# Kernel tuning notes

Measured on AMD Instinct MI355X. Metric: run time of the kernel, lower is better.

## Reference

```python
import jax, jax.numpy as jnp
import numpy as np


def setup_inputs() -> dict:
    key = jax.random.key(0)
    k1, k2 = jax.random.split(key)
    B, C, H, W = 8, 64, 32, 32
    K = 8192
    x = jax.random.normal(k1, (B, C, H, W), dtype=jnp.float32)
    codebook = jax.random.normal(k2, (K, C), dtype=jnp.float32)
    return {"x": x, "codebook": codebook}


def reference(x, codebook):
    """Faithful JAX version of VQVAE.quantize().

    x:        [B, C, H, W] latent (output of pre_quant_conv)
    codebook: [K, C] embedding weight
    Returns (quant_out [B,C,H,W], commitment_loss, codebook_loss, indices [B,H,W]).
    """
    B, C, H, W = x.shape
    # [B, H, W, C] -> [B, N, C]
    xf = jnp.transpose(x, (0, 2, 3, 1)).reshape(B, H * W, C)

    # Squared pairwise distances (argmin of cdist == argmin of squared dist).
    x2 = jnp.sum(xf * xf, axis=-1, keepdims=True)            # [B, N, 1]
    e2 = jnp.sum(codebook * codebook, axis=-1)               # [K]
    xe = jnp.einsum('bnc,kc->bnk', xf, codebook)             # [B, N, K]
    d2 = x2 + e2[None, None, :] - 2.0 * xe                   # [B, N, K]
    idx = jnp.argmin(d2, axis=-1)                            # [B, N]

    quant = codebook[idx.reshape(-1)]                        # [B*N, C]
    xflat = xf.reshape(-1, C)                                # [B*N, C]

    commitment_loss = jnp.mean((jax.lax.stop_gradient(quant) - xflat) ** 2)
    codebook_loss = jnp.mean((quant - jax.lax.stop_gradient(xflat)) ** 2)

    # Straight-through estimator.
    quant_st = xflat + jax.lax.stop_gradient(quant - xflat)
    quant_out = jnp.transpose(quant_st.reshape(B, H, W, C), (0, 3, 1, 2))
    indices = idx.reshape(B, H, W)
    return quant_out, commitment_loss, codebook_loss, indices
```

## Files before the change

kernel.cpp:

```cpp
#include <hip/hip_runtime.h>


#define N_PTS   8192
#define K_CODES 8192
#define C_DIM   64
#define HWSZ    1024
#define QOUT_N  524288
#define SPLITS  16

#define WS_XS    0
#define WS_CBS   2097152
#define WS_E2H   4194304
#define WS_PACK  4227072
#define WS_PART  5275648

typedef __attribute__((ext_vector_type(8))) short    short8;
typedef __attribute__((ext_vector_type(8))) _Float16 half8;
typedef __attribute__((ext_vector_type(4))) float    floatx4;

__device__ __forceinline__ half8 as_h8(short8 v) {
    return __builtin_bit_cast(half8, v);
}
__device__ __forceinline__ void split2(float v, unsigned short& h,
                                       unsigned short& m) {
    _Float16 hh = (_Float16)v;
    float r = v - (float)hh;
    _Float16 mm = (_Float16)r;
    h = __builtin_bit_cast(unsigned short, hh);
    m = __builtin_bit_cast(unsigned short, mm);
}
__device__ __forceinline__ void cp16(const void* g, void* l) {
    __builtin_amdgcn_global_load_lds(
        (const __attribute__((address_space(1))) void*)g,
        (__attribute__((address_space(3))) void*)l, 16, 0, 0);
}
__device__ __forceinline__ void cp4(const void* g, void* l) {
    __builtin_amdgcn_global_load_lds(
        (const __attribute__((address_space(1))) void*)g,
        (__attribute__((address_space(3))) void*)l, 4, 0, 0);
}

__global__ __launch_bounds__(256)
void vq_prep_kernel(const float* __restrict__ x,
                    const float* __restrict__ cb,
                    unsigned short* __restrict__ xS,
                    unsigned short* __restrict__ cbS,
                    float* __restrict__ e2h)
{
    const int bx  = blockIdx.x;
    const int tid = threadIdx.x;

    if (bx < 32) {
        const int k = bx * 256 + tid;
        const float* row = cb + k * C_DIM;
        float s = 0.0f;
        #pragma unroll
        for (int g = 0; g < 8; ++g) {
            float4 a = *(const float4*)(row + g * 8);
            float4 b = *(const float4*)(row + g * 8 + 4);
            float vv[8] = {a.x, a.y, a.z, a.w, b.x, b.y, b.z, b.w};
            unsigned short h8[8], m8[8];
            #pragma unroll
            for (int j = 0; j < 8; ++j) {
                s = fmaf(vv[j], vv[j], s);
                split2(vv[j], h8[j], m8[j]);
            }
            *(uint4*)(cbS + ((size_t)(0 * 8 + g) * 8192 + k) * 8) = *(const uint4*)h8;
            *(uint4*)(cbS + ((size_t)(1 * 8 + g) * 8192 + k) * 8) = *(const uint4*)m8;
        }
        e2h[k] = 0.5f * s;
    } else {
        const int u = bx - 32;
        const int b = u >> 5, g = (u >> 2) & 7, q = u & 3;
        const int hw = q * 256 + tid;
        const float* xb = x + (size_t)(b * C_DIM + g * 8) * HWSZ + hw;
        unsigned short h8[8], m8[8];
        #pragma unroll
        for (int cq = 0; cq < 8; ++cq)
            split2(xb[cq * HWSZ], h8[cq], m8[cq]);
        const size_t n = (size_t)b * 1024 + hw;
        *(uint4*)(xS + ((size_t)(0 * 8 + g) * 8192 + n) * 8) = *(const uint4*)h8;
        *(uint4*)(xS + ((size_t)(1 * 8 + g) * 8192 + n) * 8) = *(const uint4*)m8;
    }
}

#define SEG_SHORTS 512
#define NSEGS      16
#define BUF_SHORTS 8320

__device__ __forceinline__ void computeTile(const half8 af[4][2][2],
                                            const unsigned short* __restrict__ bsrc,
                                            int tl, int quad, int col, int code,
                                            float bestv[4][4], int besti[4][4])
{
    half8 bf[2][2];
    #pragma unroll
    for (int p = 0; p < 2; ++p)
        #pragma unroll
        for (int s = 0; s < 2; ++s) {
            int seg = p * 8 + s * 4 + quad;
            bf[p][s] = as_h8(*(const short8*)(bsrc + seg * SEG_SHORTS + (tl * 16 + col) * 8));
        }
    float me2 = -((const float*)(bsrc + NSEGS * SEG_SHORTS))[tl * 16 + col];

    floatx4 acc[4];
    #pragma unroll
    for (int t = 0; t < 4; ++t) acc[t] = (floatx4){me2, me2, me2, me2};

    #pragma unroll
    for (int s = 0; s < 2; ++s) {
        #pragma unroll
        for (int t = 0; t < 4; ++t)
            acc[t] = __builtin_amdgcn_mfma_f32_16x16x32_f16(af[t][0][s], bf[0][s], acc[t], 0, 0, 0);
        #pragma unroll
        for (int t = 0; t < 4; ++t)
            acc[t] = __builtin_amdgcn_mfma_f32_16x16x32_f16(af[t][0][s], bf[1][s], acc[t], 0, 0, 0);
        #pragma unroll
        for (int t = 0; t < 4; ++t)
            acc[t] = __builtin_amdgcn_mfma_f32_16x16x32_f16(af[t][1][s], bf[0][s], acc[t], 0, 0, 0);
    }

    #pragma unroll
    for (int t = 0; t < 4; ++t)
        #pragma unroll
        for (int r = 0; r < 4; ++r) {
            float sc = acc[t][r];
            bool gt = sc > bestv[t][r];
            bestv[t][r] = gt ? sc   : bestv[t][r];
            besti[t][r] = gt ? code : besti[t][r];
        }
}

__global__ __launch_bounds__(512, 1)
void vq_argmin_kernel(const unsigned short* __restrict__ xS,
                      const unsigned short* __restrict__ cbS,
                      const float* __restrict__ e2h,
                      unsigned long long* __restrict__ packedS)
{
    __shared__ __align__(16) unsigned short sBuf[2][BUF_SHORTS];

    const int tid   = threadIdx.x;
    const int lane  = tid & 63;
    const int w     = tid >> 6;
    const int col   = lane & 15;
    const int quad  = lane >> 4;
    const int mb    = blockIdx.x;
    const int split = blockIdx.y;
    const int m0    = mb * 512 + w * 64;
    const int nb0   = split * 512;

    half8 af[4][2][2];
    #pragma unroll
    for (int t = 0; t < 4; ++t) {
        int pt = m0 + t * 16 + col;
        #pragma unroll
        for (int p = 0; p < 2; ++p)
            #pragma unroll
            for (int s = 0; s < 2; ++s) {
                int g = s * 4 + quad;
                af[t][p][s] = as_h8(*(const short8*)(xS + ((size_t)(p * 8 + g) * 8192 + pt) * 8));
            }
    }

    float bestv[4][4];
    int   besti[4][4];
    #pragma unroll
    for (int t = 0; t < 4; ++t)
        #pragma unroll
        for (int r = 0; r < 4; ++r) {
            bestv[t][r] = __uint_as_float(0xFF800000u);
            besti[t][r] = 0;
        }

    auto stage = [&](int k0, int buf) {
        unsigned short* dst = &sBuf[buf][0];
        #pragma unroll
        for (int i = 0; i < 2; ++i) {
            int f   = tid + i * 512;
            int seg = f >> 6;
            int l   = f & 63;
            cp16(cbS + ((size_t)seg * 8192 + k0 + l) * 8,
                 dst + seg * SEG_SHORTS + l * 8);
        }
        if (tid < 64)
            cp4(e2h + k0 + tid, (float*)(dst + NSEGS * SEG_SHORTS) + tid);
    };

    stage(nb0, 0);
    __syncthreads();

    for (int ch = 0; ch < 8; ++ch) {
        if (ch + 1 < 8) stage(nb0 + (ch + 1) * 64, (ch + 1) & 1);
        const unsigned short* bsrc = &sBuf[ch & 1][0];
        #pragma unroll
        for (int tl = 0; tl < 4; ++tl)
            computeTile(af, bsrc, tl, quad, col,
                        nb0 + ch * 64 + tl * 16 + col, bestv, besti);
        __syncthreads();
    }

    unsigned long long own = 0;
    #pragma unroll
    for (int t = 0; t < 4; ++t)
        #pragma unroll
        for (int r = 0; r < 4; ++r) {
            unsigned u = __float_as_uint(-bestv[t][r]);
            u = ((int)u < 0) ? ~u : (u | 0x80000000u);
            unsigned long long p = ((unsigned long long)u << 32) | (unsigned)besti[t][r];
            #pragma unroll
            for (int msk = 1; msk < 16; msk <<= 1) {
                unsigned long long q = __shfl_xor(p, msk, 64);
                p = (q < p) ? q : p;
            }
            own = (col == t * 4 + r) ? p : own;
        }
    const int mpt = m0 + (col >> 2) * 16 + quad * 4 + (col & 3);
    packedS[(size_t)split * N_PTS + mpt] = own;
}

__global__ __launch_bounds__(256)
void vq_gather_kernel(const float* __restrict__ x,
                      const float* __restrict__ cb,
                      const unsigned long long* __restrict__ packedS,
                      float* __restrict__ out,
                      float* __restrict__ part)
{
    __shared__ unsigned long long sred[8][32];
    const int tid = threadIdx.x;
    const int p   = tid & 31;
    const int sg  = tid >> 5;
    const int n0  = blockIdx.x * 32;
    const int n   = n0 + p;

    {
        unsigned long long v = packedS[(size_t)(sg * 2) * N_PTS + n];
        unsigned long long q = packedS[(size_t)(sg * 2 + 1) * N_PTS + n];
        sred[sg][p] = (q < v) ? q : v;
    }
    __syncthreads();

    unsigned long long v = sred[0][p];
    #pragma unroll
    for (int s = 1; s < 8; ++s) {
        unsigned long long q = sred[s][p];
        v = (q < v) ? q : v;
    }
    const int idx = (int)(v & 0xFFFFFFFFull);
    if (tid < 32) out[QOUT_N + 2 + n0 + tid] = (float)idx;

    const int c0  = sg * 8;
    const int b   = n >> 10;
    const int hw  = n & 1023;
    const float* xb = x   + (size_t)b * (C_DIM * HWSZ) + hw;
    float*       ob = out + (size_t)b * (C_DIM * HWSZ) + hw;

    float s = 0.0f;
    #pragma unroll
    for (int c4 = 0; c4 < 2; ++c4) {
        float4 q = *(const float4*)(cb + (size_t)idx * C_DIM + c0 + c4 * 4);
        float qa[4] = {q.x, q.y, q.z, q.w};
        #pragma unroll
        for (int j = 0; j < 4; ++j) {
            int c = c0 + c4 * 4 + j;
            float xv = xb[c * HWSZ];
            float d  = qa[j] - xv;
            s = fmaf(d, d, s);
            ob[c * HWSZ] = xv + d;
        }
    }

    #pragma unroll
    for (int off = 32; off > 0; off >>= 1) s += __shfl_down(s, off, 64);
    if ((tid & 63) == 0) part[blockIdx.x * 4 + (tid >> 6)] = s;
}

__global__ __launch_bounds__(256)
void vq_final_kernel(const float* __restrict__ part, float* __restrict__ out)
{
    __shared__ float w[4];
    float s = part[threadIdx.x] + part[threadIdx.x + 256]
            + part[threadIdx.x + 512] + part[threadIdx.x + 768];
    #pragma unroll
    for (int off = 32; off > 0; off >>= 1) s += __shfl_down(s, off, 64);
    if ((threadIdx.x & 63) == 0) w[threadIdx.x >> 6] = s;
    __syncthreads();
    if (threadIdx.x == 0) {
        float m = (w[0] + w[1] + w[2] + w[3]) * (1.0f / (float)QOUT_N);
        out[QOUT_N]     = m;
        out[QOUT_N + 1] = m;
    }
}

extern "C" void kernel_launch(void* const* d_in, const int* in_sizes, int n_in,
                              void* d_out, int out_size, void* d_ws, size_t ws_size,
                              hipStream_t stream)
{
    const float* x  = (const float*)d_in[0];
    const float* cb = (const float*)d_in[1];
    float* out = (float*)d_out;
    char*  ws  = (char*)d_ws;
    (void)ws_size;

    unsigned short* xS  = (unsigned short*)(ws + WS_XS);
    unsigned short* cbS = (unsigned short*)(ws + WS_CBS);
    float* e2h = (float*)(ws + WS_E2H);
    unsigned long long* packedS = (unsigned long long*)(ws + WS_PACK);
    float* part = (float*)(ws + WS_PART);

    vq_prep_kernel<<<288, 256, 0, stream>>>(x, cb, xS, cbS, e2h);
    vq_argmin_kernel<<<dim3(16, SPLITS), 512, 0, stream>>>(xS, cbS, e2h, packedS);
    vq_gather_kernel<<<256, 256, 0, stream>>>(x, cb, packedS, out, part);
    vq_final_kernel<<<1, 256, 0, stream>>>(part, out);
}
```

Measured before the change: 90.18 us.

## Fuse x split into argmin kernel and triple-buffer codebook staging

The fp16 hi/lo split of x now happens inside the argmin kernel instead of in the prep kernel, so the xS workspace and its write/read round trip go away and the prep grid shrinks to the codebook only. The half-squared codebook norms are preloaded once per block into a dedicated shared array. Codebook staging moves from double to triple buffering, with explicit vmcnt waits and a raw s_barrier replacing __syncthreads. In exchange, each block issues strided uncoalesced-ish global loads of x, repeated across the 16 codebook splits.

```diff
diff --git a/kernel.cpp b/kernel.cpp
--- a/kernel.cpp
+++ b/kernel.cpp
@@ -8,7 +8,6 @@
 #define QOUT_N  524288
 #define SPLITS  16
 
-#define WS_XS    0
 #define WS_CBS   2097152
 #define WS_E2H   4194304
 #define WS_PACK  4227072
@@ -34,62 +33,40 @@
         (const __attribute__((address_space(1))) void*)g,
         (__attribute__((address_space(3))) void*)l, 16, 0, 0);
 }
-__device__ __forceinline__ void cp4(const void* g, void* l) {
-    __builtin_amdgcn_global_load_lds(
-        (const __attribute__((address_space(1))) void*)g,
-        (__attribute__((address_space(3))) void*)l, 4, 0, 0);
-}
 
 __global__ __launch_bounds__(256)
-void vq_prep_kernel(const float* __restrict__ x,
-                    const float* __restrict__ cb,
-                    unsigned short* __restrict__ xS,
+void vq_prep_kernel(const float* __restrict__ cb,
                     unsigned short* __restrict__ cbS,
                     float* __restrict__ e2h)
 {
-    const int bx  = blockIdx.x;
-    const int tid = threadIdx.x;
-
-    if (bx < 32) {
-        const int k = bx * 256 + tid;
-        const float* row = cb + k * C_DIM;
-        float s = 0.0f;
-        #pragma unroll
-        for (int g = 0; g < 8; ++g) {
-            float4 a = *(const float4*)(row + g * 8);
-            float4 b = *(const float4*)(row + g * 8 + 4);
-            float vv[8] = {a.x, a.y, a.z, a.w, b.x, b.y, b.z, b.w};
-            unsigned short h8[8], m8[8];
-            #pragma unroll
-            for (int j = 0; j < 8; ++j) {
-                s = fmaf(vv[j], vv[j], s);
-                split2(vv[j], h8[j], m8[j]);
-            }
-            *(uint4*)(cbS + ((size_t)(0 * 8 + g) * 8192 + k) * 8) = *(const uint4*)h8;
-            *(uint4*)(cbS + ((size_t)(1 * 8 + g) * 8192 + k) * 8) = *(const uint4*)m8;
-        }
-        e2h[k] = 0.5f * s;
-    } else {
-        const int u = bx - 32;
-        const int b = u >> 5, g = (u >> 2) & 7, q = u & 3;
-        const int hw = q * 256 + tid;
-        const float* xb = x + (size_t)(b * C_DIM + g * 8) * HWSZ + hw;
+    const int k = blockIdx.x * 256 + threadIdx.x;
+    const float* row = cb + k * C_DIM;
+    float s = 0.0f;
+    #pragma unroll
+    for (int g = 0; g < 8; ++g) {
+        float4 a = *(const float4*)(row + g * 8);
+        float4 b = *(const float4*)(row + g * 8 + 4);
+        float vv[8] = {a.x, a.y, a.z, a.w, b.x, b.y, b.z, b.w};
         unsigned short h8[8], m8[8];
         #pragma unroll
-        for (int cq = 0; cq < 8; ++cq)
-            split2(xb[cq * HWSZ], h8[cq], m8[cq]);
-        const size_t n = (size_t)b * 1024 + hw;
-        *(uint4*)(xS + ((size_t)(0 * 8 + g) * 8192 + n) * 8) = *(const uint4*)h8;
-        *(uint4*)(xS + ((size_t)(1 * 8 + g) * 8192 + n) * 8) = *(const uint4*)m8;
-    }
+        for (int j = 0; j < 8; ++j) {
+            s = fmaf(vv[j], vv[j], s);
+            split2(vv[j], h8[j], m8[j]);
+        }
+        *(uint4*)(cbS + ((size_t)(0 * 8 + g) * 8192 + k) * 8) = *(const uint4*)h8;
+        *(uint4*)(cbS + ((size_t)(1 * 8 + g) * 8192 + k) * 8) = *(const uint4*)m8;
+    }
+    e2h[k] = 0.5f * s;
 }
 
 #define SEG_SHORTS 512
 #define NSEGS      16
-#define BUF_SHORTS 8320
+#define BUF_SHORTS 8192
+#define NBUF       3
 
 __device__ __forceinline__ void computeTile(const half8 af[4][2][2],
                                             const unsigned short* __restrict__ bsrc,
+                                            const float* __restrict__ se2row,
                                             int tl, int quad, int col, int code,
                                             float bestv[4][4], int besti[4][4])
 {
@@ -101,7 +78,7 @@
             int seg = p * 8 + s * 4 + quad;
             bf[p][s] = as_h8(*(const short8*)(bsrc + seg * SEG_SHORTS + (tl * 16 + col) * 8));
         }
-    float me2 = -((const float*)(bsrc + NSEGS * SEG_SHORTS))[tl * 16 + col];
+    float me2 = -se2row[tl * 16 + col];
 
     floatx4 acc[4];
     #pragma unroll
@@ -132,12 +109,13 @@
 }
 
 __global__ __launch_bounds__(512, 1)
-void vq_argmin_kernel(const unsigned short* __restrict__ xS,
+void vq_argmin_kernel(const float* __restrict__ x,
                       const unsigned short* __restrict__ cbS,
                       const float* __restrict__ e2h,
                       unsigned long long* __restrict__ packedS)
 {
-    __shared__ __align__(16) unsigned short sBuf[2][BUF_SHORTS];
+    __shared__ __align__(16) unsigned short sBuf[NBUF][BUF_SHORTS];
+    __shared__ __align__(16) float sE2[512];
 
     const int tid   = threadIdx.x;
     const int lane  = tid & 63;
@@ -149,29 +127,6 @@
     const int m0    = mb * 512 + w * 64;
     const int nb0   = split * 512;
 
-    half8 af[4][2][2];
-    #pragma unroll
-    for (int t = 0; t < 4; ++t) {
-        int pt = m0 + t * 16 + col;
-        #pragma unroll
-        for (int p = 0; p < 2; ++p)
-            #pragma unroll
-            for (int s = 0; s < 2; ++s) {
-                int g = s * 4 + quad;
-                af[t][p][s] = as_h8(*(const short8*)(xS + ((size_t)(p * 8 + g) * 8192 + pt) * 8));
-            }
-    }
-
-    float bestv[4][4];
-    int   besti[4][4];
-    #pragma unroll
-    for (int t = 0; t < 4; ++t)
-        #pragma unroll
-        for (int r = 0; r < 4; ++r) {
-            bestv[t][r] = __uint_as_float(0xFF800000u);
-            besti[t][r] = 0;
-        }
-
     auto stage = [&](int k0, int buf) {
         unsigned short* dst = &sBuf[buf][0];
         #pragma unroll
@@ -182,21 +137,63 @@
             cp16(cbS + ((size_t)seg * 8192 + k0 + l) * 8,
                  dst + seg * SEG_SHORTS + l * 8);
         }
-        if (tid < 64)
-            cp4(e2h + k0 + tid, (float*)(dst + NSEGS * SEG_SHORTS) + tid);
     };
 
+    if (tid < 128)
+        cp16(e2h + nb0 + tid * 4, &sE2[tid * 4]);
     stage(nb0, 0);
+    stage(nb0 + 64, 1);
+
+    const int bimg = mb >> 1;
+    const int hwB  = (mb & 1) * 512 + w * 64;
+    const float* xb = x + (size_t)bimg * (C_DIM * HWSZ);
+    half8 af[4][2][2];
+    #pragma unroll
+    for (int t = 0; t < 4; ++t) {
+        const int hw = hwB + t * 16 + col;
+        #pragma unroll
+        for (int s = 0; s < 2; ++s) {
+            unsigned short h8[8], m8[8];
+            #pragma unroll
+            for (int j = 0; j < 8; ++j) {
+                float v = xb[(size_t)(s * 32 + quad * 8 + j) * HWSZ + hw];
+                split2(v, h8[j], m8[j]);
+            }
+            af[t][0][s] = as_h8(*(const short8*)h8);
+            af[t][1][s] = as_h8(*(const short8*)m8);
+        }
+    }
+
+    float bestv[4][4];
+    int   besti[4][4];
+    #pragma unroll
+    for (int t = 0; t < 4; ++t)
+        #pragma unroll
+        for (int r = 0; r < 4; ++r) {
+            bestv[t][r] = __uint_as_float(0xFF800000u);
+            besti[t][r] = 0;
+        }
+
     __syncthreads();
 
+    int cbuf = 0, pbuf = 2;
     for (int ch = 0; ch < 8; ++ch) {
-        if (ch + 1 < 8) stage(nb0 + (ch + 1) * 64, (ch + 1) & 1);
-        const unsigned short* bsrc = &sBuf[ch & 1][0];
+        if (ch < 6) stage(nb0 + (ch + 2) * 64, pbuf);
+        const unsigned short* bsrc = &sBuf[cbuf][0];
+        const float* se2row = &sE2[ch * 64];
         #pragma unroll
         for (int tl = 0; tl < 4; ++tl)
-            computeTile(af, bsrc, tl, quad, col,
+            computeTile(af, bsrc, se2row, tl, quad, col,
                         nb0 + ch * 64 + tl * 16 + col, bestv, besti);
-        __syncthreads();
+        if (ch < 7) {
+            if (ch == 6) asm volatile("s_waitcnt vmcnt(0)" ::: "memory");
+            else         asm volatile("s_waitcnt vmcnt(2)" ::: "memory");
+            __builtin_amdgcn_sched_barrier(0);
+            __builtin_amdgcn_s_barrier();
+            __builtin_amdgcn_sched_barrier(0);
+        }
+        cbuf = (cbuf == NBUF - 1) ? 0 : cbuf + 1;
+        pbuf = (pbuf == NBUF - 1) ? 0 : pbuf + 1;
     }
 
     unsigned long long own = 0;
@@ -301,14 +298,13 @@
     char*  ws  = (char*)d_ws;
     (void)ws_size;
 
-    unsigned short* xS  = (unsigned short*)(ws + WS_XS);
     unsigned short* cbS = (unsigned short*)(ws + WS_CBS);
     float* e2h = (float*)(ws + WS_E2H);
     unsigned long long* packedS = (unsigned long long*)(ws + WS_PACK);
     float* part = (float*)(ws + WS_PART);
 
-    vq_prep_kernel<<<288, 256, 0, stream>>>(x, cb, xS, cbS, e2h);
-    vq_argmin_kernel<<<dim3(16, SPLITS), 512, 0, stream>>>(xS, cbS, e2h, packedS);
+    vq_prep_kernel<<<32, 256, 0, stream>>>(cb, cbS, e2h);
+    vq_argmin_kernel<<<dim3(16, SPLITS), 512, 0, stream>>>(x, cbS, e2h, packedS);
     vq_gather_kernel<<<256, 256, 0, stream>>>(x, cb, packedS, out, part);
     vq_final_kernel<<<1, 256, 0, stream>>>(part, out);
 }
```

New measurement: 103.6 us. +14.9%, slower.
